# Performance work log

Hardware: AMD Instinct MI355X
Metric: run time of the kernel (lower is better)

## Reference

```python
import jax, jax.numpy as jnp
import numpy as np

D = 256  # hardcoded Dense units in the original layer

def setup_inputs() -> dict:
    key = jax.random.key(0)
    ks = jax.random.split(key, 7)
    B, S, F = 8, 2048, 256
    x = jax.random.normal(ks[0], (B, S, F), dtype=jnp.float32)
    # Dense layers (kernel + bias), glorot-ish scale
    scale = 1.0 / np.sqrt(F)
    Wq = jax.random.normal(ks[1], (F, D), dtype=jnp.float32) * scale
    Wk = jax.random.normal(ks[2], (F, D), dtype=jnp.float32) * scale
    Wv = jax.random.normal(ks[3], (F, D), dtype=jnp.float32) * scale
    bq = jax.random.normal(ks[4], (D,), dtype=jnp.float32) * 0.01
    bk = jax.random.normal(ks[5], (D,), dtype=jnp.float32) * 0.01
    bv = jax.random.normal(ks[6], (D,), dtype=jnp.float32) * 0.01
    return {"x": x, "Wq": Wq, "bq": bq, "Wk": Wk, "bk": bk, "Wv": Wv, "bv": bv}

def reference(x, Wq, bq, Wk, bk, Wv, bv):
    # Q/K/V projections: Dense(256) == x @ W + b
    Q = jnp.einsum('bsf,fd->bsd', x, Wq) + bq
    K = jnp.einsum('bsf,fd->bsd', x, Wk) + bk
    V = jnp.einsum('bsf,fd->bsd', x, Wv) + bv
    scores = jnp.einsum('bqd,bkd->bqk', Q, K) / jnp.sqrt(jnp.float32(D))
    attn = jax.nn.softmax(scores, axis=-1)
    return jnp.einsum('bqk,bkd->bqd', attn, V)
```

## Files before the change

### kernel.cpp

```cpp
#include <hip/hip_runtime.h>

typedef __bf16 bf16;
typedef __bf16 bf16x4v __attribute__((ext_vector_type(4)));
typedef __bf16 bf16x8 __attribute__((ext_vector_type(8)));
typedef float f32x4 __attribute__((ext_vector_type(4)));
typedef short s16x4 __attribute__((ext_vector_type(4)));

#define MFMA_X32(A, B, C) __builtin_amdgcn_mfma_f32_16x16x32_bf16(A, B, C, 0, 0, 0)

static __device__ __forceinline__ float fast_exp2(float x) {
  float r;
  asm volatile("v_exp_f32 %0, %1\n\ts_nop 0" : "=v"(r) : "v"(x));
  return r;
}

static __device__ __forceinline__ void gll16(const void* g, void* l) {
  __builtin_amdgcn_global_load_lds(
      (const __attribute__((address_space(1))) void*)g,
      (__attribute__((address_space(3))) void*)l, 16, 0, 0);
}

#define WT_OFF 0
#define Q_OFF 393216
#define K_OFF 8781824
#define V_OFF 17170432

__global__ __launch_bounds__(256) void prep_wt(const float* __restrict__ Wq,
                                               const float* __restrict__ Wk,
                                               const float* __restrict__ Wv,
                                               bf16* __restrict__ Wt) {
  const int idx = blockIdx.x * 256 + threadIdx.x;
  const int p = idx >> 16;
  const int rem = idx & 65535;
  const int k = rem >> 8, n = rem & 255;
  const float* W = (p == 0) ? Wq : ((p == 1) ? Wk : Wv);
  Wt[p * 65536 + n * 256 + k] = (bf16)W[rem];
}

__global__ __launch_bounds__(256, 3) void proj_qkv(const float* __restrict__ x,
                                                   const float* __restrict__ bq,
                                                   const float* __restrict__ bk,
                                                   const float* __restrict__ bv,
                                                   char* __restrict__ ws0) {
  __shared__ __align__(16) char smem[40960];
  const bf16* Wt = (const bf16*)(ws0 + WT_OFF);
  bf16* Qo = (bf16*)(ws0 + Q_OFF);
  bf16* Ko = (bf16*)(ws0 + K_OFF);
  bf16* Vc = (bf16*)(ws0 + V_OFF);
  const int t = threadIdx.x;
  const int lane = t & 63, w = t >> 6, l16 = lane & 15, quad = lane >> 4;
  const int fam = blockIdx.x % 6;
  const int rgroup = blockIdx.x / 6;
  const int p = fam >> 1, ch = fam & 1;
  const float* bias = (p == 0) ? bq : ((p == 1) ? bk : bv);
  const float sc = (p == 0) ? 0.09016844005556021f : 1.0f;

  const int nl = w * 32 + l16;
  bf16x8 bfr[2][8];
#pragma unroll
  for (int nt = 0; nt < 2; ++nt)
#pragma unroll
    for (int kt = 0; kt < 8; ++kt)
      bfr[nt][kt] = *(const bf16x8*)&Wt[p * 65536 + (ch * 128 + nl + nt * 16) * 256 +
                                        kt * 32 + quad * 8];
  float bias2[2];
#pragma unroll
  for (int nt = 0; nt < 2; ++nt) bias2[nt] = bias[ch * 128 + nl + nt * 16];

  const int row0 = rgroup * 128;
  char* outL = smem + 32768;

  float4 xr[4][2];
#define STAGE_LOAD(tile)                                                        \
  {                                                                             \
    const float* xp = x + (row0 + (tile) * 32) * 256;                           \
    _Pragma("unroll") for (int i = 0; i < 4; ++i) {                             \
      const int u2 = i * 256 + t, row = u2 >> 5, col8 = (u2 & 31) * 8;          \
      xr[i][0] = *(const float4*)&xp[row * 256 + col8];                         \
      xr[i][1] = *(const float4*)&xp[row * 256 + col8 + 4];                     \
    }                                                                           \
  }
#define STAGE_WRITE(buf)                                                        \
  {                                                                             \
    _Pragma("unroll") for (int i = 0; i < 4; ++i) {                             \
      const int u2 = i * 256 + t, row = u2 >> 5, col8 = (u2 & 31) * 8;          \
      const float* f0 = (const float*)&xr[i][0];                                \
      const float* f1 = (const float*)&xr[i][1];                                \
      bf16x8 h;                                                                 \
      _Pragma("unroll") for (int j = 0; j < 4; ++j) {                           \
        h[j] = (bf16)f0[j];                                                     \
        h[4 + j] = (bf16)f1[j];                                                 \
      }                                                                         \
      *(bf16x8*)&smem[(buf) * 16384 + row * 512 +                               \
                      ((col8 * 2) ^ ((row & 7) << 4))] = h;                     \
    }                                                                           \
  }

  STAGE_LOAD(0);
  STAGE_WRITE(0);
  __syncthreads();

  int cur = 0;
  for (int tt = 0; tt < 4; ++tt) {
    if (tt < 3) STAGE_LOAD(tt + 1);

    f32x4 acc[2][2];
#pragma unroll
    for (int rs = 0; rs < 2; ++rs)
#pragma unroll
      for (int nt = 0; nt < 2; ++nt) acc[rs][nt] = f32x4{0.f, 0.f, 0.f, 0.f};
    const char* xb = smem + cur * 16384;
#pragma unroll
    for (int rs = 0; rs < 2; ++rs) {
      const int row = rs * 16 + l16;
#pragma unroll
      for (int kt = 0; kt < 8; ++kt) {
        const bf16x8 a = *(const bf16x8*)(xb + row * 512 +
                                          ((kt * 64 + quad * 16) ^ ((l16 & 7) << 4)));
        acc[rs][0] = MFMA_X32(a, bfr[0][kt], acc[rs][0]);
        acc[rs][1] = MFMA_X32(a, bfr[1][kt], acc[rs][1]);
      }
    }
    __syncthreads();

#pragma unroll
    for (int rs = 0; rs < 2; ++rs)
#pragma unroll
      for (int nt = 0; nt < 2; ++nt)
#pragma unroll
        for (int r = 0; r < 4; ++r) {
          const int sl = rs * 16 + quad * 4 + r;
          const int nn = nl + nt * 16;
          const bf16 hv = (bf16)((acc[rs][nt][r] + bias2[nt]) * sc);
          int pos;
          if (p == 0)
            pos = sl * 128 + nn;
          else if (p == 1)
            pos = (sl >> 4) * 2048 + (nn >> 5) * 512 + ((nn >> 3) & 3) * 128 +
                  (sl & 15) * 8 + (nn & 7);
          else
            pos = (nn >> 4) * 512 + ((sl >> 2) & 3) * 128 + (nn & 15) * 8 +
                  (sl >> 4) * 4 + (sl & 3);
          *(bf16*)(outL + pos * 2) = hv;
        }
    if (tt < 3) STAGE_WRITE(cur ^ 1);
    __syncthreads();

    const int rowg = row0 + tt * 32;
    if (p == 0) {
      const int row = t >> 3, cb = (t & 7) * 32;
      const float4 v0 = *(const float4*)(outL + row * 256 + cb);
      const float4 v1 = *(const float4*)(outL + row * 256 + cb + 16);
      char* dst = (char*)Qo + (rowg + row) * 512 + ch * 256 + cb;
      *(float4*)dst = v0;
      *(float4*)(dst + 16) = v1;
    } else if (p == 1) {
      const int b2 = rowg >> 11, s0 = rowg & 2047;
      char* dst = (char*)Ko + b2 * 1048576 + ((s0 >> 4) + (t >> 7)) * 8192 +
                  ch * 4096 + (t & 127) * 32;
      const float4 v0 = *(const float4*)(outL + t * 32);
      const float4 v1 = *(const float4*)(outL + t * 32 + 16);
      *(float4*)dst = v0;
      *(float4*)(dst + 16) = v1;
    } else {
      const int b2 = rowg >> 11, s0 = rowg & 2047;
      char* dst = (char*)Vc + b2 * 1048576 + (s0 >> 5) * 16384 + ch * 8192 + t * 32;
      const float4 v0 = *(const float4*)(outL + t * 32);
      const float4 v1 = *(const float4*)(outL + t * 32 + 16);
      *(float4*)dst = v0;
      *(float4*)(dst + 16) = v1;
    }
    cur ^= 1;
  }
#undef STAGE_LOAD
#undef STAGE_WRITE
}

#define SLOT_SZ 16640

__global__ __launch_bounds__(512, 2) void flash_attn(const char* __restrict__ ws0,
                                                     float* __restrict__ out) {
  __shared__ __align__(1024) char smem[135168];
  const bf16* Qp = (const bf16*)(ws0 + Q_OFF);
  const int t = threadIdx.x;
  const int lane = t & 63, w = t >> 6;
  const int l16 = lane & 15, quad = lane >> 4;
  const int qs = w & 1, kq = w >> 1;
  const int b = blockIdx.x & 7;
  const int qt = blockIdx.x >> 3;
  const int qrow0 = b * 2048 + qt * 64 + qs * 32;

  bf16x8 qf[2][8];
#pragma unroll
  for (int qsub = 0; qsub < 2; ++qsub)
#pragma unroll
    for (int kt = 0; kt < 8; ++kt)
      qf[qsub][kt] =
          *(const bf16x8*)&Qp[(qrow0 + qsub * 16 + l16) * 256 + kt * 32 + quad * 8];

  f32x4 o[2][16];
#pragma unroll
  for (int qsub = 0; qsub < 2; ++qsub)
#pragma unroll
    for (int dt = 0; dt < 16; ++dt) o[qsub][dt] = f32x4{0.f, 0.f, 0.f, 0.f};
  float m_[2] = {-1e30f, -1e30f}, l_[2] = {0.f, 0.f};

  unsigned goffK[4], loffK[4];
#pragma unroll
  for (int i = 0; i < 4; ++i) {
    const int u = w * 4 + i;
    const int kq2 = u >> 3, e = u & 7;
    goffK[i] = (unsigned)K_OFF + b * 1048576u + kq2 * 262144u + e * 1024u + lane * 16u;
    loffK[i] = kq2 * 8192u + e * 1024u;
  }
  unsigned goffV[8], loffV[8];
#pragma unroll
  for (int i = 0; i < 8; ++i) {
    const int u = w * 8 + i;
    const int kqv = u >> 4, e = u & 15;
    goffV[i] = (unsigned)V_OFF + b * 1048576u + kqv * 262144u + e * 1024u + lane * 16u;
    loffV[i] = 65536u + kqv * 16384u + e * 1024u;
  }

#define STAGE_K(S)                                                             \
  {                                                                            \
    _Pragma("unroll") for (int i = 0; i < 4; ++i)                              \
        gll16(ws0 + goffK[i] + (unsigned)(S) * 8192u,                          \
              smem + (unsigned)(((S) & 1) * 32768) + loffK[i]);                \
  }
#define STAGE_V(P)                                                             \
  {                                                                            \
    _Pragma("unroll") for (int i = 0; i < 8; ++i)                              \
        gll16(ws0 + goffV[i] + (unsigned)(P) * 16384u, smem + loffV[i]);       \
  }
#define QK_STEP(CURK, KC)                                                      \
  {                                                                            \
    const char* kb = smem + (CURK) + kq * 8192 + lane * 16;                    \
    __builtin_amdgcn_s_setprio(1);                                             \
    _Pragma("unroll") for (int kt = 0; kt < 8; ++kt) {                         \
      const bf16x8 kf = *(const bf16x8*)(kb + kt * 1024);                      \
      sfr[0][KC] = MFMA_X32(kf, qf[0][kt], sfr[0][KC]);                        \
      sfr[1][KC] = MFMA_X32(kf, qf[1][kt], sfr[1][KC]);                        \
    }                                                                          \
    __builtin_amdgcn_s_setprio(0);                                             \
  }

  STAGE_K(0);

  for (int p = 0; p < 16; ++p) {
    f32x4 sfr[2][2];
#pragma unroll
    for (int qsub = 0; qsub < 2; ++qsub)
#pragma unroll
      for (int kc = 0; kc < 2; ++kc) sfr[qsub][kc] = f32x4{0.f, 0.f, 0.f, 0.f};

    __syncthreads();
    STAGE_K(2 * p + 1);
    STAGE_V(p);
    QK_STEP((unsigned)((2 * p) & 1) * 32768u, 0);

    __syncthreads();
    if (p < 15) STAGE_K(2 * p + 2);
    QK_STEP((unsigned)((2 * p + 1) & 1) * 32768u, 1);

    bf16x8 pa[2];
#pragma unroll
    for (int qsub = 0; qsub < 2; ++qsub) {
      const f32x4 sA = sfr[qsub][0], sB = sfr[qsub][1];
      float cm = fmaxf(fmaxf(fmaxf(sA[0], sA[1]), fmaxf(sA[2], sA[3])),
                       fmaxf(fmaxf(sB[0], sB[1]), fmaxf(sB[2], sB[3])));
      cm = fmaxf(cm, __shfl_xor(cm, 16));
      cm = fmaxf(cm, __shfl_xor(cm, 32));
      const float mold = m_[qsub];
      const bool upd = __any(cm > mold + 6.0f);
      float Mref = mold;
      if (upd) Mref = fmaxf(mold, cm);
      float ps = 0.f;
#pragma unroll
      for (int r = 0; r < 4; ++r) {
        const bf16 p0 = (bf16)fast_exp2(sA[r] - Mref);
        const bf16 p1 = (bf16)fast_exp2(sB[r] - Mref);
        pa[qsub][r] = p0;
        pa[qsub][4 + r] = p1;
        ps += (float)p0 + (float)p1;
      }
      ps += __shfl_xor(ps, 16);
      ps += __shfl_xor(ps, 32);
      if (upd) {
        const float al = fast_exp2(mold - Mref);
        m_[qsub] = Mref;
        l_[qsub] = l_[qsub] * al + ps;
        float ar[4];
#pragma unroll
        for (int r = 0; r < 4; ++r)
          ar[r] = __shfl(al, (quad << 4) + (quad << 2) + r);
#pragma unroll
        for (int dt = 0; dt < 16; ++dt)
#pragma unroll
          for (int r = 0; r < 4; ++r) o[qsub][dt][r] *= ar[r];
      } else {
        l_[qsub] += ps;
      }
    }

    const char* vb = smem + 65536 + kq * 16384 + lane * 16;
    __builtin_amdgcn_s_setprio(1);
#pragma unroll
    for (int dt = 0; dt < 16; ++dt) {
      const bf16x8 vf = *(const bf16x8*)(vb + dt * 1024);
      o[0][dt] = MFMA_X32(pa[0], vf, o[0][dt]);
      o[1][dt] = MFMA_X32(pa[1], vf, o[1][dt]);
    }
    __builtin_amdgcn_s_setprio(0);
  }
#undef STAGE_K
#undef STAGE_V
#undef QK_STEP

  float* mlf = (float*)(smem + 133120);
  if (quad == 0) {
#pragma unroll
    for (int qsub = 0; qsub < 2; ++qsub) {
      const int base = ((kq * 2 + qs) * 2 + qsub) * 32;
      mlf[base + l16] = m_[qsub];
      mlf[base + 16 + l16] = l_[qsub];
    }
  }
  __syncthreads();
#pragma unroll
  for (int qsub = 0; qsub < 2; ++qsub) {
    float M = -1e30f, mk[4], lk[4];
#pragma unroll
    for (int k2 = 0; k2 < 4; ++k2) {
      const int base = ((k2 * 2 + qs) * 2 + qsub) * 32;
      mk[k2] = mlf[base + l16];
      lk[k2] = mlf[base + 16 + l16];
      M = fmaxf(M, mk[k2]);
    }
    float L = 0.f;
#pragma unroll
    for (int k2 = 0; k2 < 4; ++k2) L += lk[k2] * fast_exp2(mk[k2] - M);
    const float sg = fast_exp2(m_[qsub] - M) / L;
    float sr[4];
#pragma unroll
    for (int r = 0; r < 4; ++r) sr[r] = __shfl(sg, (quad << 4) + (quad << 2) + r);
#pragma unroll
    for (int dt = 0; dt < 16; ++dt)
#pragma unroll
      for (int r = 0; r < 4; ++r) o[qsub][dt][r] *= sr[r];
  }
  if (kq >= 2) {
#pragma unroll
    for (int qsub = 0; qsub < 2; ++qsub) {
      float* sb = (float*)(smem + ((kq - 2) * 4 + qs * 2 + qsub) * SLOT_SZ);
#pragma unroll
      for (int dt = 0; dt < 16; ++dt)
#pragma unroll
        for (int r = 0; r < 4; ++r)
          sb[(quad * 4 + r) * 260 + dt * 16 + l16] = o[qsub][dt][r];
    }
  }
  __syncthreads();
  if (kq < 2) {
#pragma unroll
    for (int qsub = 0; qsub < 2; ++qsub) {
      const float* sb = (const float*)(smem + (kq * 4 + qs * 2 + qsub) * SLOT_SZ);
#pragma unroll
      for (int dt = 0; dt < 16; ++dt)
#pragma unroll
        for (int r = 0; r < 4; ++r)
          o[qsub][dt][r] += sb[(quad * 4 + r) * 260 + dt * 16 + l16];
    }
  }
  __syncthreads();
  if (kq == 1) {
#pragma unroll
    for (int qsub = 0; qsub < 2; ++qsub) {
      float* sb = (float*)(smem + (qs * 2 + qsub) * SLOT_SZ);
#pragma unroll
      for (int dt = 0; dt < 16; ++dt)
#pragma unroll
        for (int r = 0; r < 4; ++r)
          sb[(quad * 4 + r) * 260 + dt * 16 + l16] = o[qsub][dt][r];
    }
  }
  __syncthreads();
  if (kq == 0) {
#pragma unroll
    for (int qsub = 0; qsub < 2; ++qsub) {
      const float* sb = (const float*)(smem + (qs * 2 + qsub) * SLOT_SZ);
#pragma unroll
      for (int dt = 0; dt < 16; ++dt)
#pragma unroll
        for (int r = 0; r < 4; ++r) {
          const float v = o[qsub][dt][r] + sb[(quad * 4 + r) * 260 + dt * 16 + l16];
          out[(qrow0 + qsub * 16 + quad * 4 + r) * 256 + dt * 16 + l16] = v;
        }
    }
  }
}

extern "C" void kernel_launch(void* const* d_in, const int* in_sizes, int n_in,
                              void* d_out, int out_size, void* d_ws,
                              size_t ws_size, hipStream_t stream) {
  const float* x = (const float*)d_in[0];
  const float* Wq = (const float*)d_in[1];
  const float* bq = (const float*)d_in[2];
  const float* Wk = (const float*)d_in[3];
  const float* bk = (const float*)d_in[4];
  const float* Wv = (const float*)d_in[5];
  const float* bv = (const float*)d_in[6];
  float* out = (float*)d_out;
  char* ws = (char*)d_ws;

  prep_wt<<<768, 256, 0, stream>>>(Wq, Wk, Wv, (bf16*)(ws + WT_OFF));
  proj_qkv<<<768, 256, 0, stream>>>(x, bq, bk, bv, ws);
  flash_attn<<<256, 512, 0, stream>>>(ws, out);
}
```

Before: 164.0 us.

## Triple-buffer K tiles with explicit vmcnt waits to deepen prefetch

Moves the K staging from a double buffer to three rotating LDS buffers, so K tiles are prefetched two steps ahead. Full `__syncthreads` calls are replaced by `s_waitcnt vmcnt(N)` plus a raw barrier, so only the loads actually needed are waited on. The goal is to hide global-to-LDS latency behind the QK MFMAs. LDS per block grows to 160 KB, which likely allows only one 512-thread block per CU instead of the two requested by the launch bounds. A final barrier is added because the m/l scratch area now overlaps the V buffer.

```diff
diff --git a/kernel.cpp b/kernel.cpp
--- a/kernel.cpp
+++ b/kernel.cpp
@@ -19,6 +19,13 @@
       (const __attribute__((address_space(1))) void*)g,
       (__attribute__((address_space(3))) void*)l, 16, 0, 0);
 }
+
+#define WAIT_BARRIER(N)                                        \
+  {                                                            \
+    asm volatile("s_waitcnt vmcnt(" #N ")" ::: "memory");      \
+    __builtin_amdgcn_s_barrier();                              \
+    asm volatile("" ::: "memory");                             \
+  }
 
 #define WT_OFF 0
 #define Q_OFF 393216
@@ -176,11 +183,13 @@
 #undef STAGE_WRITE
 }
 
+#define KBUFSZ 32768u
+#define VBASE 98304u
 #define SLOT_SZ 16640
 
 __global__ __launch_bounds__(512, 2) void flash_attn(const char* __restrict__ ws0,
                                                      float* __restrict__ out) {
-  __shared__ __align__(1024) char smem[135168];
+  __shared__ __align__(1024) char smem[163840];
   const bf16* Qp = (const bf16*)(ws0 + Q_OFF);
   const int t = threadIdx.x;
   const int lane = t & 63, w = t >> 6;
@@ -219,23 +228,23 @@
     const int u = w * 8 + i;
     const int kqv = u >> 4, e = u & 15;
     goffV[i] = (unsigned)V_OFF + b * 1048576u + kqv * 262144u + e * 1024u + lane * 16u;
-    loffV[i] = 65536u + kqv * 16384u + e * 1024u;
-  }
-
-#define STAGE_K(S)                                                             \
+    loffV[i] = kqv * 16384u + e * 1024u;
+  }
+
+#define STAGE_K(S, BUF)                                                        \
   {                                                                            \
     _Pragma("unroll") for (int i = 0; i < 4; ++i)                              \
         gll16(ws0 + goffK[i] + (unsigned)(S) * 8192u,                          \
-              smem + (unsigned)(((S) & 1) * 32768) + loffK[i]);                \
+              smem + (unsigned)(BUF) * KBUFSZ + loffK[i]);                     \
   }
 #define STAGE_V(P)                                                             \
   {                                                                            \
     _Pragma("unroll") for (int i = 0; i < 8; ++i)                              \
-        gll16(ws0 + goffV[i] + (unsigned)(P) * 16384u, smem + loffV[i]);       \
-  }
-#define QK_STEP(CURK, KC)                                                      \
+        gll16(ws0 + goffV[i] + (unsigned)(P) * 16384u, smem + VBASE + loffV[i]); \
+  }
+#define QK_STEP(BUF, KC)                                                       \
   {                                                                            \
-    const char* kb = smem + (CURK) + kq * 8192 + lane * 16;                    \
+    const char* kb = smem + (unsigned)(BUF) * KBUFSZ + kq * 8192 + lane * 16;  \
     __builtin_amdgcn_s_setprio(1);                                             \
     _Pragma("unroll") for (int kt = 0; kt < 8; ++kt) {                         \
       const bf16x8 kf = *(const bf16x8*)(kb + kt * 1024);                      \
@@ -245,8 +254,10 @@
     __builtin_amdgcn_s_setprio(0);                                             \
   }
 
-  STAGE_K(0);
-
+  STAGE_K(0, 0);
+  STAGE_K(1, 1);
+
+  int b0 = 0, b1 = 1, b2 = 2;
   for (int p = 0; p < 16; ++p) {
     f32x4 sfr[2][2];
 #pragma unroll
@@ -254,14 +265,23 @@
 #pragma unroll
       for (int kc = 0; kc < 2; ++kc) sfr[qsub][kc] = f32x4{0.f, 0.f, 0.f, 0.f};
 
-    __syncthreads();
-    STAGE_K(2 * p + 1);
+    if (p == 0) {
+      WAIT_BARRIER(0)
+    } else {
+      WAIT_BARRIER(4)
+    }
     STAGE_V(p);
-    QK_STEP((unsigned)((2 * p) & 1) * 32768u, 0);
-
-    __syncthreads();
-    if (p < 15) STAGE_K(2 * p + 2);
-    QK_STEP((unsigned)((2 * p + 1) & 1) * 32768u, 1);
+    asm volatile("" ::: "memory");
+    if (p < 15) STAGE_K(2 * p + 2, b2);
+    QK_STEP(b0, 0);
+
+    if (p < 15) {
+      WAIT_BARRIER(4)
+      STAGE_K(2 * p + 3, b0);
+    } else {
+      WAIT_BARRIER(0)
+    }
+    QK_STEP(b1, 1);
 
     bf16x8 pa[2];
 #pragma unroll
@@ -303,7 +323,7 @@
       }
     }
 
-    const char* vb = smem + 65536 + kq * 16384 + lane * 16;
+    const char* vb = smem + VBASE + kq * 16384 + lane * 16;
     __builtin_amdgcn_s_setprio(1);
 #pragma unroll
     for (int dt = 0; dt < 16; ++dt) {
@@ -312,10 +332,17 @@
       o[1][dt] = MFMA_X32(pa[1], vf, o[1][dt]);
     }
     __builtin_amdgcn_s_setprio(0);
+
+    const int nb0 = b2, nb1 = b0, nb2 = b1;
+    b0 = nb0;
+    b1 = nb1;
+    b2 = nb2;
   }
 #undef STAGE_K
 #undef STAGE_V
 #undef QK_STEP
+
+  __syncthreads();
 
   float* mlf = (float*)(smem + 133120);
   if (quad == 0) {
```

Result: slower. 200.5 us (+22.3%).

## Load V fragments directly from global into registers, double-buffer K pairs in LDS

Applied to the files above, without the earlier changes.

V tiles are no longer staged through LDS; each wave loads its V fragments straight from global memory into registers, with the loads interleaved across the PV MFMA loop. K is now staged two tiles at a time into a double-buffered 64KB LDS region, cutting the per-iteration barriers from two to one. The wave index is made scalar via readfirstlane. This trades LDS traffic and a barrier for higher register pressure (16 extra bf16x8 registers) and more exposed global-load latency on V.

```diff
diff --git a/kernel.cpp b/kernel.cpp
--- a/kernel.cpp
+++ b/kernel.cpp
@@ -183,7 +183,8 @@
   __shared__ __align__(1024) char smem[135168];
   const bf16* Qp = (const bf16*)(ws0 + Q_OFF);
   const int t = threadIdx.x;
-  const int lane = t & 63, w = t >> 6;
+  const int lane = t & 63;
+  const int w = __builtin_amdgcn_readfirstlane(t >> 6);
   const int l16 = lane & 15, quad = lane >> 4;
   const int qs = w & 1, kq = w >> 1;
   const int b = blockIdx.x & 7;
@@ -205,63 +206,62 @@
     for (int dt = 0; dt < 16; ++dt) o[qsub][dt] = f32x4{0.f, 0.f, 0.f, 0.f};
   float m_[2] = {-1e30f, -1e30f}, l_[2] = {0.f, 0.f};
 
-  unsigned goffK[4], loffK[4];
+  const unsigned lane16 = (unsigned)lane * 16u;
+  unsigned gK[4], lK[4];
 #pragma unroll
   for (int i = 0; i < 4; ++i) {
     const int u = w * 4 + i;
     const int kq2 = u >> 3, e = u & 7;
-    goffK[i] = (unsigned)K_OFF + b * 1048576u + kq2 * 262144u + e * 1024u + lane * 16u;
-    loffK[i] = kq2 * 8192u + e * 1024u;
-  }
-  unsigned goffV[8], loffV[8];
-#pragma unroll
-  for (int i = 0; i < 8; ++i) {
-    const int u = w * 8 + i;
-    const int kqv = u >> 4, e = u & 15;
-    goffV[i] = (unsigned)V_OFF + b * 1048576u + kqv * 262144u + e * 1024u + lane * 16u;
-    loffV[i] = 65536u + kqv * 16384u + e * 1024u;
-  }
-
-#define STAGE_K(S)                                                             \
+    gK[i] = (unsigned)K_OFF + (unsigned)b * 1048576u + (unsigned)kq2 * 262144u +
+            (unsigned)e * 1024u;
+    lK[i] = (unsigned)kq2 * 8192u + (unsigned)e * 1024u;
+  }
+  const char* vg0 = ws0 + (unsigned)V_OFF + (unsigned)b * 1048576u +
+                    (unsigned)kq * 262144u + lane16;
+
+#define STAGE_PAIR(Q)                                                          \
   {                                                                            \
-    _Pragma("unroll") for (int i = 0; i < 4; ++i)                              \
-        gll16(ws0 + goffK[i] + (unsigned)(S) * 8192u,                          \
-              smem + (unsigned)(((S) & 1) * 32768) + loffK[i]);                \
-  }
-#define STAGE_V(P)                                                             \
+    _Pragma("unroll") for (int h = 0; h < 2; ++h)                              \
+        _Pragma("unroll") for (int i = 0; i < 4; ++i)                          \
+        gll16(ws0 + gK[i] + (unsigned)(2 * (Q) + h) * 8192u + lane16,          \
+              smem + (unsigned)((Q) & 1) * 65536u + (unsigned)h * 32768u +     \
+                  lK[i]);                                                      \
+  }
+#define QK_STEP(KOFFB, KC)                                                     \
   {                                                                            \
-    _Pragma("unroll") for (int i = 0; i < 8; ++i)                              \
-        gll16(ws0 + goffV[i] + (unsigned)(P) * 16384u, smem + loffV[i]);       \
-  }
-#define QK_STEP(CURK, KC)                                                      \
-  {                                                                            \
-    const char* kb = smem + (CURK) + kq * 8192 + lane * 16;                    \
     __builtin_amdgcn_s_setprio(1);                                             \
     _Pragma("unroll") for (int kt = 0; kt < 8; ++kt) {                         \
-      const bf16x8 kf = *(const bf16x8*)(kb + kt * 1024);                      \
+      const bf16x8 kf = *(const bf16x8*)(kb + (KOFFB) + kt * 1024);            \
       sfr[0][KC] = MFMA_X32(kf, qf[0][kt], sfr[0][KC]);                        \
       sfr[1][KC] = MFMA_X32(kf, qf[1][kt], sfr[1][KC]);                        \
     }                                                                          \
     __builtin_amdgcn_s_setprio(0);                                             \
   }
 
-  STAGE_K(0);
+  STAGE_PAIR(0);
 
   for (int p = 0; p < 16; ++p) {
+    __syncthreads();
+    const char* kb = smem + (unsigned)(p & 1) * 65536u + (unsigned)kq * 8192u +
+                     lane16;
+    const char* vg = vg0 + (unsigned)p * 16384u;
+
+    bf16x8 vr[16];
+#pragma unroll
+    for (int dt = 0; dt < 4; ++dt)
+      vr[dt] = *(const bf16x8*)(vg + dt * 1024);
+#pragma unroll
+    for (int dt = 4; dt < 8; ++dt)
+      vr[dt] = *(const bf16x8*)(vg + dt * 1024);
+    if (p < 15) STAGE_PAIR(p + 1);
+
     f32x4 sfr[2][2];
 #pragma unroll
     for (int qsub = 0; qsub < 2; ++qsub)
 #pragma unroll
       for (int kc = 0; kc < 2; ++kc) sfr[qsub][kc] = f32x4{0.f, 0.f, 0.f, 0.f};
-
-    __syncthreads();
-    STAGE_K(2 * p + 1);
-    STAGE_V(p);
-    QK_STEP((unsigned)((2 * p) & 1) * 32768u, 0);
-
-    __syncthreads();
-    if (p < 15) STAGE_K(2 * p + 2);
-    QK_STEP((unsigned)((2 * p + 1) & 1) * 32768u, 1);
+    QK_STEP(0, 0);
+    QK_STEP(32768, 1);
 
     bf16x8 pa[2];
 #pragma unroll
@@ -303,19 +303,39 @@
       }
     }
 
-    const char* vb = smem + 65536 + kq * 16384 + lane * 16;
     __builtin_amdgcn_s_setprio(1);
 #pragma unroll
-    for (int dt = 0; dt < 16; ++dt) {
-      const bf16x8 vf = *(const bf16x8*)(vb + dt * 1024);
-      o[0][dt] = MFMA_X32(pa[0], vf, o[0][dt]);
-      o[1][dt] = MFMA_X32(pa[1], vf, o[1][dt]);
+    for (int dt = 0; dt < 4; ++dt) {
+      o[0][dt] = MFMA_X32(pa[0], vr[dt], o[0][dt]);
+      o[1][dt] = MFMA_X32(pa[1], vr[dt], o[1][dt]);
+    }
+#pragma unroll
+    for (int dt = 8; dt < 12; ++dt)
+      vr[dt] = *(const bf16x8*)(vg + dt * 1024);
+#pragma unroll
+    for (int dt = 4; dt < 8; ++dt) {
+      o[0][dt] = MFMA_X32(pa[0], vr[dt], o[0][dt]);
+      o[1][dt] = MFMA_X32(pa[1], vr[dt], o[1][dt]);
+    }
+#pragma unroll
+    for (int dt = 12; dt < 16; ++dt)
+      vr[dt] = *(const bf16x8*)(vg + dt * 1024);
+#pragma unroll
+    for (int dt = 8; dt < 12; ++dt) {
+      o[0][dt] = MFMA_X32(pa[0], vr[dt], o[0][dt]);
+      o[1][dt] = MFMA_X32(pa[1], vr[dt], o[1][dt]);
+    }
+#pragma unroll
+    for (int dt = 12; dt < 16; ++dt) {
+      o[0][dt] = MFMA_X32(pa[0], vr[dt], o[0][dt]);
+      o[1][dt] = MFMA_X32(pa[1], vr[dt], o[1][dt]);
     }
     __builtin_amdgcn_s_setprio(0);
   }
-#undef STAGE_K
-#undef STAGE_V
+#undef STAGE_PAIR
 #undef QK_STEP
+
+  __syncthreads();
 
   float* mlf = (float*)(smem + 133120);
   if (quad == 0) {
```

Result: slower. 186.9 us (+14.0%).
